# Performance work log

Measured on AMD Instinct MI355X. Metric: run time of the kernel, lower is better.

## Reference

```python
import jax, jax.numpy as jnp
import numpy as np

D_MODEL = 1024
HEADS = 16
D_K = D_MODEL // HEADS
B, S = 4, 2048


def setup_inputs() -> dict:
    key = jax.random.key(0)
    ks = jax.random.split(key, 12)
    xav = float(np.sqrt(6.0 / (D_MODEL + D_MODEL)))  # xavier_uniform bound
    inp = {
        "query": jax.random.normal(ks[0], (B, S, D_MODEL), jnp.float32),
        "key": jax.random.normal(ks[1], (B, S, D_MODEL), jnp.float32),
        "value": jax.random.normal(ks[2], (B, S, D_MODEL), jnp.float32),
        # causal mask, broadcast over batch and heads: [1,1,S,S]
        "mask": jnp.tril(jnp.ones((S, S), jnp.int32))[None, None],
        "Wq": jax.random.uniform(ks[3], (D_MODEL, D_MODEL), jnp.float32, -xav, xav),
        "bq": jnp.zeros((D_MODEL,), jnp.float32),
        "Wk": jax.random.uniform(ks[4], (D_MODEL, D_MODEL), jnp.float32, -xav, xav),
        "bk": jnp.zeros((D_MODEL,), jnp.float32),
        "Wv": jax.random.uniform(ks[5], (D_MODEL, D_MODEL), jnp.float32, -xav, xav),
        "bv": jnp.zeros((D_MODEL,), jnp.float32),
        "Wo": jax.random.uniform(ks[6], (D_MODEL, D_MODEL), jnp.float32, -xav, xav),
        "bo": jnp.zeros((D_MODEL,), jnp.float32),
    }
    return inp


def reference(query, key, value, mask, Wq, bq, Wk, bk, Wv, bv, Wo, bo):
    b, s, d = query.shape
    # torch Linear: y = x @ W.T + b, W is [out, in]
    Q = (jnp.einsum("bsd,ed->bse", query, Wq) + bq).reshape(b, s, HEADS, D_K).transpose(0, 2, 1, 3)
    K = (jnp.einsum("bsd,ed->bse", key, Wk) + bk).reshape(b, -1, HEADS, D_K).transpose(0, 2, 1, 3)
    V = (jnp.einsum("bsd,ed->bse", value, Wv) + bv).reshape(b, -1, HEADS, D_K).transpose(0, 2, 1, 3)
    scale = 1.0 / jnp.sqrt(jnp.asarray(D_K, query.dtype))
    scores = jnp.einsum("bhqd,bhkd->bhqk", Q, K) * scale  # [B,H,S,S]
    scores = jnp.where(mask == 0, -jnp.inf, scores)
    attn = jax.nn.softmax(scores, axis=-1)
    attn = jnp.where(jnp.isnan(attn), jnp.zeros_like(attn), attn)  # nan-fix as in source
    out = jnp.einsum("bhqk,bhkd->bhqd", attn, V)
    out = out.transpose(0, 2, 1, 3).reshape(b, s, d)
    return jnp.einsum("bsd,ed->bse", out, Wo) + bo
```

## Files before the change

### kernel.cpp

```cpp
#include <hip/hip_runtime.h>
#include <hip/hip_bf16.h>

#define DM 1024
#define NHEADS 16
#define DKH 64
#define BATCH 4
#define SEQ 2048
#define MROWS (BATCH*SEQ)

typedef __attribute__((ext_vector_type(8))) short bf16x8;
typedef __attribute__((ext_vector_type(4))) short bf16x4;
typedef __attribute__((ext_vector_type(4))) float f32x4;

#if __has_builtin(__builtin_amdgcn_exp2f)
#define EXP2(x) __builtin_amdgcn_exp2f(x)
#else
#define EXP2(x) exp2f(x)
#endif

__device__ __forceinline__ unsigned short f2bf(float f){
  unsigned u = __float_as_uint(f);
  u += 0x7fffu + ((u >> 16) & 1u);
  return (unsigned short)(u >> 16);
}

__device__ __forceinline__ unsigned pk2bf(float lo, float hi){
  union { __hip_bfloat162 h; unsigned u; } c;
  c.h = __float22bfloat162_rn(make_float2(lo, hi));
  return c.u;
}

__device__ __forceinline__ bf16x8 cvtA8(float4 a, float4 b){
  union { unsigned u[4]; bf16x8 v; } r;
  r.u[0] = pk2bf(a.x, a.y);
  r.u[1] = pk2bf(a.z, a.w);
  r.u[2] = pk2bf(b.x, b.y);
  r.u[3] = pk2bf(b.z, b.w);
  return r.v;
}

__device__ __forceinline__ void gload16(const unsigned short* g, unsigned short* l){
  __builtin_amdgcn_global_load_lds((const __attribute__((address_space(1))) void*)g,
                                   (__attribute__((address_space(3))) void*)l, 16, 0, 0);
}

struct ConvArgs { const float* src[4]; unsigned short* dst[4]; };

__global__ __launch_bounds__(256) void conv_w(ConvArgs a){
  const int t = blockIdx.x >> 10;
  const int boff = blockIdx.x & 1023;
  const float* __restrict__ src = a.src[t];
  unsigned short* __restrict__ dst = a.dst[t];
  const int i = (boff * 256 + threadIdx.x) * 4;
  const float4 v = *reinterpret_cast<const float4*>(src + i);
  ushort4 o;
  o.x = f2bf(v.x); o.y = f2bf(v.y); o.z = f2bf(v.z); o.w = f2bf(v.w);
  *reinterpret_cast<ushort4*>(dst + i) = o;
}

template<int MODE, int AFP32>
__global__ __launch_bounds__(256)
void gemm_bt(const void* __restrict__ Av, const unsigned short* __restrict__ Bw,
             const float* __restrict__ bias, void* __restrict__ out, float scale)
{
  const int K = 1024;
  __shared__ short a_sh[128*64];
  __shared__ short b_sh[128*64];
  const int tid  = threadIdx.x;
  const int lane = tid & 63;
  const int wid  = tid >> 6;
  const int wm = wid >> 1, wn = wid & 1;
  const int lin = blockIdx.x;
  const int xcd = lin & 7;
  const int i9  = lin >> 3;
  const int tileM = (8*xcd + (i9 >> 3)) * 128;
  const int tileN = (i9 & 7) * 128;

  f32x4 acc[4][4];
  #pragma unroll
  for (int i = 0; i < 4; i++)
    #pragma unroll
    for (int j = 0; j < 4; j++)
      acc[i][j] = (f32x4){0.f,0.f,0.f,0.f};

  const int lr = lane & 15;
  const int lg = lane >> 4;
  const int r8 = lane >> 3, c8 = lane & 7;
  const int srow = 8*wid + r8;
  const int sgrp = (c8 ^ r8) * 8;

  for (int k0 = 0; k0 < K; k0 += 64){
    bf16x8 ra[4];
    if constexpr (AFP32){
      const float* Af = (const float*)Av;
      #pragma unroll
      for (int i = 0; i < 4; i++){
        int v   = tid + 256*i;
        int row = v >> 3;
        int cg  = v & 7;
        const float4 f0 = *reinterpret_cast<const float4*>(Af + (size_t)(tileM+row)*K + k0 + cg*8);
        const float4 f1 = *reinterpret_cast<const float4*>(Af + (size_t)(tileM+row)*K + k0 + cg*8 + 4);
        ra[i] = cvtA8(f0, f1);
      }
    }
    __syncthreads();
    #pragma unroll
    for (int j = 0; j < 4; j++){
      gload16(Bw + (size_t)(tileN + srow + 32*j)*K + k0 + sgrp,
              (unsigned short*)&b_sh[(8*wid + 32*j)*64]);
    }
    if constexpr (AFP32){
      #pragma unroll
      for (int i = 0; i < 4; i++){
        int v   = tid + 256*i;
        int row = v >> 3;
        int cg  = v & 7;
        *reinterpret_cast<bf16x8*>(&a_sh[row*64 + ((cg ^ (row & 7)) * 8)]) = ra[i];
      }
    } else {
      const unsigned short* Ab = (const unsigned short*)Av;
      #pragma unroll
      for (int j = 0; j < 4; j++){
        gload16(Ab + (size_t)(tileM + srow + 32*j)*K + k0 + sgrp,
                (unsigned short*)&a_sh[(8*wid + 32*j)*64]);
      }
    }
    __syncthreads();

    #pragma unroll
    for (int kk = 0; kk < 64; kk += 32){
      bf16x8 af[4], bfr[4];
      const int g0 = lg + (kk >> 3);
      #pragma unroll
      for (int fm = 0; fm < 4; fm++){
        int row = wm*64 + fm*16 + lr;
        af[fm] = *reinterpret_cast<const bf16x8*>(&a_sh[row*64 + ((g0 ^ (row & 7)) * 8)]);
      }
      #pragma unroll
      for (int fn = 0; fn < 4; fn++){
        int row = wn*64 + fn*16 + lr;
        bfr[fn] = *reinterpret_cast<const bf16x8*>(&b_sh[row*64 + ((g0 ^ (row & 7)) * 8)]);
      }
      #pragma unroll
      for (int fm = 0; fm < 4; fm++)
        #pragma unroll
        for (int fn = 0; fn < 4; fn++)
          acc[fm][fn] = __builtin_amdgcn_mfma_f32_16x16x32_bf16(af[fm], bfr[fn], acc[fm][fn], 0, 0, 0);
    }
  }

  #pragma unroll
  for (int fm = 0; fm < 4; fm++){
    #pragma unroll
    for (int fn = 0; fn < 4; fn++){
      #pragma unroll
      for (int r = 0; r < 4; r++){
        int m = tileM + wm*64 + fm*16 + lg*4 + r;
        int n = tileN + wn*64 + fn*16 + lr;
        float val = acc[fm][fn][r] + bias[n];
        if (MODE == 0){
          val *= scale;
          int b = m >> 11, s = m & 2047, h = n >> 6, d = n & 63;
          ((unsigned short*)out)[(((size_t)(b*NHEADS + h)*SEQ + s)*DKH + d)] = f2bf(val);
        } else if (MODE == 1){
          int b = m >> 11, s = m & 2047, h = n >> 6, d = n & 63;
          ((unsigned short*)out)[(((size_t)(b*NHEADS + h)*DKH + d)*SEQ + s)] = f2bf(val);
        } else {
          ((float*)out)[(size_t)m*DM + n] = val;
        }
      }
    }
  }
}

__global__ __launch_bounds__(512, 4)
void attn_kernel(const unsigned short* __restrict__ Q, const unsigned short* __restrict__ Kb,
                 const unsigned short* __restrict__ Vt, unsigned short* __restrict__ Oout)
{
  __shared__ unsigned short k_sh[2][64*64];
  __shared__ unsigned short v_sh[2][64*64];
  const int lane = threadIdx.x & 63;
  const int w    = threadIdx.x >> 6;
  const int lr = lane & 15, grp = lane >> 4;
  const int bh = blockIdx.x;
  const int y  = (int)blockIdx.y;
  const int hiT = 15 - y;
  const int myTile = (w < 4) ? hiT : y;
  const int qb0 = myTile * 128;
  const int qw0 = qb0 + (w & 3) * 32;
  const int b = bh >> 4, h = bh & 15;
  const size_t kbase = (size_t)bh * SEQ * DKH;
  const size_t vbase = (size_t)bh * DKH * SEQ;

  const int r8 = lane >> 3, c8 = lane & 7;
  const int rowS = 8*w + r8;
  const size_t offK = (size_t)rowS*DKH + (size_t)((c8 ^ r8) * 8);
  const size_t offV = (size_t)rowS*SEQ + (size_t)((c8 ^ r8) * 8);
  const int ldsOf = (8*w)*64;

  bf16x8 qf[2][2];
  #pragma unroll
  for (int qg = 0; qg < 2; qg++){
    size_t off = kbase + (size_t)(qw0 + qg*16 + lr)*DKH + grp*8;
    qf[qg][0] = *reinterpret_cast<const bf16x8*>(Q + off);
    qf[qg][1] = *reinterpret_cast<const bf16x8*>(Q + off + 32);
  }

  bf16x4 ones4;
  ones4[0] = (short)0x3F80; ones4[1] = (short)0x3F80;
  ones4[2] = (short)0x3F80; ones4[3] = (short)0x3F80;

  float mrun[2] = {-__builtin_inff(), -__builtin_inff()};
  f32x4 ls[2];
  f32x4 o[2][4];
  #pragma unroll
  for (int qg = 0; qg < 2; qg++){
    ls[qg] = (f32x4){0.f,0.f,0.f,0.f};
    #pragma unroll
    for (int dc = 0; dc < 4; dc++) o[qg][dc] = (f32x4){0.f,0.f,0.f,0.f};
  }

  const int nkb = 2*hiT + 2;

#define STAGE(kb_, bf_) do { \
    gload16(Kb + kbase + (size_t)(kb_)*4096 + offK, (unsigned short*)&k_sh[bf_][ldsOf]); \
    gload16(Vt + vbase + (size_t)(kb_)*64   + offV, (unsigned short*)&v_sh[bf_][ldsOf]); \
  } while(0)

  STAGE(0, 0);
  __syncthreads();

  for (int kb = 0; kb < nkb; kb++){
    const int buf = kb & 1;
    if (kb + 1 < nkb) STAGE(kb + 1, buf ^ 1);

    if (kb*64 <= qw0 + 31){
      const unsigned short* ks = k_sh[buf];
      const unsigned short* vs = v_sh[buf];
      const bool act0 = (kb*64 <= qw0 + 15);

      bf16x4 pb[2][4];
      #pragma unroll
      for (int qg = 0; qg < 2; qg++){
        if (qg == 0 && !act0) continue;
        f32x4 st[4];
        __builtin_amdgcn_s_setprio(1);
        #pragma unroll
        for (int ksub = 0; ksub < 4; ksub++){
          int rowk = ksub*16 + lr;
          bf16x8 kf0 = *reinterpret_cast<const bf16x8*>(&ks[rowk*64 + ((grp ^ (rowk & 7)) * 8)]);
          bf16x8 kf1 = *reinterpret_cast<const bf16x8*>(&ks[rowk*64 + (((4 + grp) ^ (rowk & 7)) * 8)]);
          f32x4 s = (f32x4){0.f,0.f,0.f,0.f};
          s = __builtin_amdgcn_mfma_f32_16x16x32_bf16(kf0, qf[qg][0], s, 0, 0, 0);
          s = __builtin_amdgcn_mfma_f32_16x16x32_bf16(kf1, qf[qg][1], s, 0, 0, 0);
          st[ksub] = s;
        }
        __builtin_amdgcn_s_setprio(0);

        const int qgb = qw0 + qg*16;
        if (kb*64 + 63 > qgb){
          #pragma unroll
          for (int ksub = 0; ksub < 4; ksub++)
            #pragma unroll
            for (int r = 0; r < 4; r++){
              int kg = kb*64 + ksub*16 + grp*4 + r;
              if (kg > qgb + lr) st[ksub][r] = -__builtin_inff();
            }
        }
        float mt = fmaxf(fmaxf(st[0][0], st[0][1]), fmaxf(st[0][2], st[0][3]));
        #pragma unroll
        for (int ksub = 1; ksub < 4; ksub++){
          mt = fmaxf(mt, fmaxf(fmaxf(st[ksub][0], st[ksub][1]),
                               fmaxf(st[ksub][2], st[ksub][3])));
        }
        mt = fmaxf(mt, __shfl_xor(mt, 16));
        mt = fmaxf(mt, __shfl_xor(mt, 32));
        const float mnew = fmaxf(mrun[qg], mt);
        const float corr = EXP2(mrun[qg] - mnew);
        mrun[qg] = mnew;
        #pragma unroll
        for (int dc = 0; dc < 4; dc++){
          o[qg][dc][0] *= corr; o[qg][dc][1] *= corr;
          o[qg][dc][2] *= corr; o[qg][dc][3] *= corr;
        }
        ls[qg][0] *= corr;
        #pragma unroll
        for (int ksub = 0; ksub < 4; ksub++){
          float p0 = EXP2(st[ksub][0] - mnew);
          float p1 = EXP2(st[ksub][1] - mnew);
          float p2 = EXP2(st[ksub][2] - mnew);
          float p3 = EXP2(st[ksub][3] - mnew);
          union { unsigned u[2]; bf16x4 v; } pk;
          pk.u[0] = pk2bf(p0, p1);
          pk.u[1] = pk2bf(p2, p3);
          pb[qg][ksub] = pk.v;
        }
      }

      __builtin_amdgcn_s_setprio(1);
      #pragma unroll
      for (int ksub = 0; ksub < 4; ksub++){
        #pragma unroll
        for (int dc = 0; dc < 4; dc++){
          int rowd = dc*16 + lr;
          int cg16 = ksub*2 + (grp >> 1);
          bf16x4 vf = *reinterpret_cast<const bf16x4*>(
              &vs[rowd*64 + ((cg16 ^ (rowd & 7)) * 8) + (grp & 1)*4]);
          if (act0) o[0][dc] = __builtin_amdgcn_mfma_f32_16x16x16bf16_1k(vf, pb[0][ksub], o[0][dc], 0, 0, 0);
          o[1][dc] = __builtin_amdgcn_mfma_f32_16x16x16bf16_1k(vf, pb[1][ksub], o[1][dc], 0, 0, 0);
        }
        if (act0) ls[0] = __builtin_amdgcn_mfma_f32_16x16x16bf16_1k(ones4, pb[0][ksub], ls[0], 0, 0, 0);
        ls[1] = __builtin_amdgcn_mfma_f32_16x16x16bf16_1k(ones4, pb[1][ksub], ls[1], 0, 0, 0);
      }
      __builtin_amdgcn_s_setprio(0);
    }
    __syncthreads();
  }
#undef STAGE

  #pragma unroll
  for (int qg = 0; qg < 2; qg++){
    float inv = 1.0f / ls[qg][0];
    int qglob = qw0 + qg*16 + lr;
    size_t ob = ((size_t)(b*SEQ + qglob))*DM + h*DKH;
    #pragma unroll
    for (int dc = 0; dc < 4; dc++){
      ushort4 pk;
      pk.x = f2bf(o[qg][dc][0]*inv);
      pk.y = f2bf(o[qg][dc][1]*inv);
      pk.z = f2bf(o[qg][dc][2]*inv);
      pk.w = f2bf(o[qg][dc][3]*inv);
      *reinterpret_cast<ushort4*>(&Oout[ob + dc*16 + grp*4]) = pk;
    }
  }
}

extern "C" void kernel_launch(void* const* d_in, const int* in_sizes, int n_in,
                              void* d_out, int out_size, void* d_ws, size_t ws_size,
                              hipStream_t stream) {
  const float* query = (const float*)d_in[0];
  const float* key   = (const float*)d_in[1];
  const float* value = (const float*)d_in[2];
  const float* Wq = (const float*)d_in[4];
  const float* bq = (const float*)d_in[5];
  const float* Wk = (const float*)d_in[6];
  const float* bk = (const float*)d_in[7];
  const float* Wv = (const float*)d_in[8];
  const float* bv = (const float*)d_in[9];
  const float* Wo = (const float*)d_in[10];
  const float* bo = (const float*)d_in[11];
  float* out = (float*)d_out;

  char* ws = (char*)d_ws;
  const size_t SZ_X = (size_t)MROWS * DM * 2;
  const size_t SZ_W = (size_t)DM * DM * 2;
  unsigned short* wqb = (unsigned short*)(ws + 0);
  unsigned short* wkb = (unsigned short*)(ws + SZ_W);
  unsigned short* wvb = (unsigned short*)(ws + 2*SZ_W);
  unsigned short* wob = (unsigned short*)(ws + 3*SZ_W);
  unsigned short* Qb   = (unsigned short*)(ws + 4*SZ_W);
  unsigned short* Kbuf = (unsigned short*)(ws + 4*SZ_W + SZ_X);
  unsigned short* Vt   = (unsigned short*)(ws + 4*SZ_W + 2*SZ_X);
  unsigned short* attO = (unsigned short*)(ws + 4*SZ_W + 3*SZ_X);

  ConvArgs ca;
  ca.src[0] = Wq; ca.src[1] = Wk; ca.src[2] = Wv; ca.src[3] = Wo;
  ca.dst[0] = wqb; ca.dst[1] = wkb; ca.dst[2] = wvb; ca.dst[3] = wob;
  conv_w<<<4096, 256, 0, stream>>>(ca);

  const int NBLK = (MROWS/128) * (DM/128);
  const float qscale = 0.125f * 1.4426950408889634f;
  gemm_bt<1,1><<<NBLK, 256, 0, stream>>>(value, wvb, bv, (void*)Vt,   1.0f);
  gemm_bt<0,1><<<NBLK, 256, 0, stream>>>(query, wqb, bq, (void*)Qb,   qscale);
  gemm_bt<0,1><<<NBLK, 256, 0, stream>>>(key,   wkb, bk, (void*)Kbuf, 1.0f);

  attn_kernel<<<dim3(64, 8), 512, 0, stream>>>(Qb, Kbuf, Vt, attO);

  gemm_bt<2,0><<<NBLK, 256, 0, stream>>>(attO, wob, bo, (void*)out, 1.0f);
}
```

Baseline: 197.6 us.

## Double K/V tile to 128 keys per barrier and add lazy softmax rescaling

Each staged tile now holds 128 keys split into two 64-key halves processed inside one iteration, which halves the number of block-wide barriers and stage rounds in the attention loop. The V swizzle is rewritten for 128-wide rows. The online softmax now skips the max update and accumulator rescale unless the new max exceeds the running max by more than 8 (log2 units), which saves multiplies and exp work but allows probabilities up to 2^8 before normalisation. LDS use doubles, which can lower occupancy.

```diff
diff --git a/kernel.cpp b/kernel.cpp
--- a/kernel.cpp
+++ b/kernel.cpp
@@ -177,8 +177,8 @@
 void attn_kernel(const unsigned short* __restrict__ Q, const unsigned short* __restrict__ Kb,
                  const unsigned short* __restrict__ Vt, unsigned short* __restrict__ Oout)
 {
-  __shared__ unsigned short k_sh[2][64*64];
-  __shared__ unsigned short v_sh[2][64*64];
+  __shared__ unsigned short k_sh[2][128*64];
+  __shared__ unsigned short v_sh[2][64*128];
   const int lane = threadIdx.x & 63;
   const int w    = threadIdx.x >> 6;
   const int lr = lane & 15, grp = lane >> 4;
@@ -193,10 +193,13 @@
   const size_t vbase = (size_t)bh * DKH * SEQ;
 
   const int r8 = lane >> 3, c8 = lane & 7;
-  const int rowS = 8*w + r8;
-  const size_t offK = (size_t)rowS*DKH + (size_t)((c8 ^ r8) * 8);
-  const size_t offV = (size_t)rowS*SEQ + (size_t)((c8 ^ r8) * 8);
-  const int ldsOf = (8*w)*64;
+  const size_t offK0 = (size_t)(16*w + r8)*DKH     + (size_t)((c8 ^ r8) * 8);
+  const size_t offK1 = (size_t)(16*w + 8 + r8)*DKH + (size_t)((c8 ^ r8) * 8);
+  const int ldsK0 = (16*w)*64, ldsK1 = (16*w + 8)*64;
+  const int r4 = lane >> 4, c16 = lane & 15;
+  const size_t offV0 = (size_t)(8*w + r4)*SEQ     + (size_t)((c16 ^ r4) * 8);
+  const size_t offV1 = (size_t)(8*w + 4 + r4)*SEQ + (size_t)((c16 ^ (4 + r4)) * 8);
+  const int ldsV0 = (8*w)*128, ldsV1 = (8*w + 4)*128;
 
   bf16x8 qf[2][2];
   #pragma unroll
@@ -220,11 +223,13 @@
     for (int dc = 0; dc < 4; dc++) o[qg][dc] = (f32x4){0.f,0.f,0.f,0.f};
   }
 
-  const int nkb = 2*hiT + 2;
+  const int nkb = hiT + 1;
 
 #define STAGE(kb_, bf_) do { \
-    gload16(Kb + kbase + (size_t)(kb_)*4096 + offK, (unsigned short*)&k_sh[bf_][ldsOf]); \
-    gload16(Vt + vbase + (size_t)(kb_)*64   + offV, (unsigned short*)&v_sh[bf_][ldsOf]); \
+    gload16(Kb + kbase + (size_t)(kb_)*8192 + offK0, (unsigned short*)&k_sh[bf_][ldsK0]); \
+    gload16(Kb + kbase + (size_t)(kb_)*8192 + offK1, (unsigned short*)&k_sh[bf_][ldsK1]); \
+    gload16(Vt + vbase + (size_t)(kb_)*128  + offV0, (unsigned short*)&v_sh[bf_][ldsV0]); \
+    gload16(Vt + vbase + (size_t)(kb_)*128  + offV1, (unsigned short*)&v_sh[bf_][ldsV1]); \
   } while(0)
 
   STAGE(0, 0);
@@ -234,85 +239,93 @@
     const int buf = kb & 1;
     if (kb + 1 < nkb) STAGE(kb + 1, buf ^ 1);
 
-    if (kb*64 <= qw0 + 31){
-      const unsigned short* ks = k_sh[buf];
-      const unsigned short* vs = v_sh[buf];
-      const bool act0 = (kb*64 <= qw0 + 15);
-
-      bf16x4 pb[2][4];
-      #pragma unroll
-      for (int qg = 0; qg < 2; qg++){
-        if (qg == 0 && !act0) continue;
-        f32x4 st[4];
+    #pragma unroll
+    for (int kh = 0; kh < 2; kh++){
+      const int base_k = kb*128 + kh*64;
+      if (base_k <= qw0 + 31){
+        const unsigned short* ks = &k_sh[buf][kh*4096];
+        const unsigned short* vs = v_sh[buf];
+        const bool act0 = (base_k <= qw0 + 15);
+
+        bf16x4 pb[2][4];
+        #pragma unroll
+        for (int qg = 0; qg < 2; qg++){
+          if (qg == 0 && !act0) continue;
+          f32x4 st[4];
+          __builtin_amdgcn_s_setprio(1);
+          #pragma unroll
+          for (int ksub = 0; ksub < 4; ksub++){
+            int rowk = ksub*16 + lr;
+            bf16x8 kf0 = *reinterpret_cast<const bf16x8*>(&ks[rowk*64 + ((grp ^ (rowk & 7)) * 8)]);
+            bf16x8 kf1 = *reinterpret_cast<const bf16x8*>(&ks[rowk*64 + (((4 + grp) ^ (rowk & 7)) * 8)]);
+            f32x4 s = (f32x4){0.f,0.f,0.f,0.f};
+            s = __builtin_amdgcn_mfma_f32_16x16x32_bf16(kf0, qf[qg][0], s, 0, 0, 0);
+            s = __builtin_amdgcn_mfma_f32_16x16x32_bf16(kf1, qf[qg][1], s, 0, 0, 0);
+            st[ksub] = s;
+          }
+          __builtin_amdgcn_s_setprio(0);
+
+          const int qgb = qw0 + qg*16;
+          if (base_k + 63 > qgb){
+            #pragma unroll
+            for (int ksub = 0; ksub < 4; ksub++)
+              #pragma unroll
+              for (int r = 0; r < 4; r++){
+                int kg = base_k + ksub*16 + grp*4 + r;
+                if (kg > qgb + lr) st[ksub][r] = -__builtin_inff();
+              }
+          }
+          float mt = fmaxf(fmaxf(st[0][0], st[0][1]), fmaxf(st[0][2], st[0][3]));
+          #pragma unroll
+          for (int ksub = 1; ksub < 4; ksub++){
+            mt = fmaxf(mt, fmaxf(fmaxf(st[ksub][0], st[ksub][1]),
+                                 fmaxf(st[ksub][2], st[ksub][3])));
+          }
+          mt = fmaxf(mt, __shfl_xor(mt, 16));
+          mt = fmaxf(mt, __shfl_xor(mt, 32));
+          if (__any(mt > mrun[qg] + 8.f)){
+            const float mold = mrun[qg];
+            const float mnew = fmaxf(mold, mt);
+            const float corr = EXP2(mold - mnew);
+            mrun[qg] = mnew;
+            #pragma unroll
+            for (int dc = 0; dc < 4; dc++){
+              o[qg][dc][0] *= corr; o[qg][dc][1] *= corr;
+              o[qg][dc][2] *= corr; o[qg][dc][3] *= corr;
+            }
+            ls[qg][0] *= corr;
+          }
+          const float m = mrun[qg];
+          #pragma unroll
+          for (int ksub = 0; ksub < 4; ksub++){
+            float p0 = EXP2(st[ksub][0] - m);
+            float p1 = EXP2(st[ksub][1] - m);
+            float p2 = EXP2(st[ksub][2] - m);
+            float p3 = EXP2(st[ksub][3] - m);
+            union { unsigned u[2]; bf16x4 v; } pk;
+            pk.u[0] = pk2bf(p0, p1);
+            pk.u[1] = pk2bf(p2, p3);
+            pb[qg][ksub] = pk.v;
+          }
+        }
+
         __builtin_amdgcn_s_setprio(1);
         #pragma unroll
         for (int ksub = 0; ksub < 4; ksub++){
-          int rowk = ksub*16 + lr;
-          bf16x8 kf0 = *reinterpret_cast<const bf16x8*>(&ks[rowk*64 + ((grp ^ (rowk & 7)) * 8)]);
-          bf16x8 kf1 = *reinterpret_cast<const bf16x8*>(&ks[rowk*64 + (((4 + grp) ^ (rowk & 7)) * 8)]);
-          f32x4 s = (f32x4){0.f,0.f,0.f,0.f};
-          s = __builtin_amdgcn_mfma_f32_16x16x32_bf16(kf0, qf[qg][0], s, 0, 0, 0);
-          s = __builtin_amdgcn_mfma_f32_16x16x32_bf16(kf1, qf[qg][1], s, 0, 0, 0);
-          st[ksub] = s;
+          const int cg16 = kh*8 + ksub*2 + (grp >> 1);
+          #pragma unroll
+          for (int dc = 0; dc < 4; dc++){
+            int rowd = dc*16 + lr;
+            bf16x4 vf = *reinterpret_cast<const bf16x4*>(
+                &vs[rowd*128 + ((cg16 ^ (rowd & 7)) * 8) + (grp & 1)*4]);
+            if (act0) o[0][dc] = __builtin_amdgcn_mfma_f32_16x16x16bf16_1k(vf, pb[0][ksub], o[0][dc], 0, 0, 0);
+            o[1][dc] = __builtin_amdgcn_mfma_f32_16x16x16bf16_1k(vf, pb[1][ksub], o[1][dc], 0, 0, 0);
+          }
+          if (act0) ls[0] = __builtin_amdgcn_mfma_f32_16x16x16bf16_1k(ones4, pb[0][ksub], ls[0], 0, 0, 0);
+          ls[1] = __builtin_amdgcn_mfma_f32_16x16x16bf16_1k(ones4, pb[1][ksub], ls[1], 0, 0, 0);
         }
         __builtin_amdgcn_s_setprio(0);
-
-        const int qgb = qw0 + qg*16;
-        if (kb*64 + 63 > qgb){
-          #pragma unroll
-          for (int ksub = 0; ksub < 4; ksub++)
-            #pragma unroll
-            for (int r = 0; r < 4; r++){
-              int kg = kb*64 + ksub*16 + grp*4 + r;
-              if (kg > qgb + lr) st[ksub][r] = -__builtin_inff();
-            }
-        }
-        float mt = fmaxf(fmaxf(st[0][0], st[0][1]), fmaxf(st[0][2], st[0][3]));
-        #pragma unroll
-        for (int ksub = 1; ksub < 4; ksub++){
-          mt = fmaxf(mt, fmaxf(fmaxf(st[ksub][0], st[ksub][1]),
-                               fmaxf(st[ksub][2], st[ksub][3])));
-        }
-        mt = fmaxf(mt, __shfl_xor(mt, 16));
-        mt = fmaxf(mt, __shfl_xor(mt, 32));
-        const float mnew = fmaxf(mrun[qg], mt);
-        const float corr = EXP2(mrun[qg] - mnew);
-        mrun[qg] = mnew;
-        #pragma unroll
-        for (int dc = 0; dc < 4; dc++){
-          o[qg][dc][0] *= corr; o[qg][dc][1] *= corr;
-          o[qg][dc][2] *= corr; o[qg][dc][3] *= corr;
-        }
-        ls[qg][0] *= corr;
-        #pragma unroll
-        for (int ksub = 0; ksub < 4; ksub++){
-          float p0 = EXP2(st[ksub][0] - mnew);
-          float p1 = EXP2(st[ksub][1] - mnew);
-          float p2 = EXP2(st[ksub][2] - mnew);
-          float p3 = EXP2(st[ksub][3] - mnew);
-          union { unsigned u[2]; bf16x4 v; } pk;
-          pk.u[0] = pk2bf(p0, p1);
-          pk.u[1] = pk2bf(p2, p3);
-          pb[qg][ksub] = pk.v;
-        }
-      }
-
-      __builtin_amdgcn_s_setprio(1);
-      #pragma unroll
-      for (int ksub = 0; ksub < 4; ksub++){
-        #pragma unroll
-        for (int dc = 0; dc < 4; dc++){
-          int rowd = dc*16 + lr;
-          int cg16 = ksub*2 + (grp >> 1);
-          bf16x4 vf = *reinterpret_cast<const bf16x4*>(
-              &vs[rowd*64 + ((cg16 ^ (rowd & 7)) * 8) + (grp & 1)*4]);
-          if (act0) o[0][dc] = __builtin_amdgcn_mfma_f32_16x16x16bf16_1k(vf, pb[0][ksub], o[0][dc], 0, 0, 0);
-          o[1][dc] = __builtin_amdgcn_mfma_f32_16x16x16bf16_1k(vf, pb[1][ksub], o[1][dc], 0, 0, 0);
-        }
-        if (act0) ls[0] = __builtin_amdgcn_mfma_f32_16x16x16bf16_1k(ones4, pb[0][ksub], ls[0], 0, 0, 0);
-        ls[1] = __builtin_amdgcn_mfma_f32_16x16x16bf16_1k(ones4, pb[1][ksub], ls[1], 0, 0, 0);
-      }
-      __builtin_amdgcn_s_setprio(0);
+      }
     }
     __syncthreads();
   }
```

Measured after the change: 193.1 us. 2.3% less time.
